# Kernel tuning notes

Hardware: AMD Instinct MI355X
Metric: run time of the kernel (lower is better)

Reference implementation:

```python
import jax, jax.numpy as jnp
import numpy as np

N = 50000      # nodes
E = 800000     # edges
DIM = 64       # node feature dim (= out_channels per head)
H = 4          # attention heads
EDGE_DIM = 3
LN_EPS = 1e-5
SLOPE = 0.2    # leaky relu negative slope (GATv2 default and FFN)


def _ln(x, g, b):
    mu = jnp.mean(x, axis=-1, keepdims=True)
    var = jnp.mean(jnp.square(x - mu), axis=-1, keepdims=True)
    return (x - mu) * jax.lax.rsqrt(var + LN_EPS) * g + b


def setup_inputs() -> dict:
    key = jax.random.key(0)
    ks = jax.random.split(key, 10)
    def g(k, shape, s=0.05):
        return jax.random.normal(k, shape, dtype=jnp.float32) * s
    return {
        "x": g(ks[0], (N, DIM), 1.0),
        "edge_index": jax.random.randint(ks[1], (2, E), 0, N),
        "edge_attr": g(ks[2], (E, EDGE_DIM), 1.0),
        # GATv2Conv params (lin_l, lin_r with bias; lin_edge no bias; att; out bias)
        "Wl": g(ks[3], (DIM, H * DIM)), "bl": jnp.zeros((H * DIM,), jnp.float32),
        "Wr": g(ks[4], (DIM, H * DIM)), "br": jnp.zeros((H * DIM,), jnp.float32),
        "We": g(ks[5], (EDGE_DIM, H * DIM)),
        "att_w": g(ks[6], (H, DIM)),
        "gat_b": jnp.zeros((DIM,), jnp.float32),
        # LayerNorms
        "ln1_g": jnp.ones((DIM,), jnp.float32), "ln1_b": jnp.zeros((DIM,), jnp.float32),
        "ln2_g": jnp.ones((DIM,), jnp.float32), "ln2_b": jnp.zeros((DIM,), jnp.float32),
        # FFN
        "W1": g(ks[7], (DIM, 2 * DIM)), "b1": jnp.zeros((2 * DIM,), jnp.float32),
        "W2": g(ks[8], (2 * DIM, DIM)), "b2": jnp.zeros((DIM,), jnp.float32),
    }


def _gatv2(x, edge_index, edge_attr, Wl, bl, Wr, br, We, att_w, gat_b):
    n = x.shape[0]
    src, dst = edge_index[0], edge_index[1]
    # add self loops; edge_attr fill_value='mean' (PyG default): per-target mean
    ea_sum = jax.ops.segment_sum(edge_attr, dst, num_segments=n)
    cnt = jax.ops.segment_sum(jnp.ones((edge_attr.shape[0], 1), edge_attr.dtype), dst, num_segments=n)
    loop_attr = ea_sum / jnp.maximum(cnt, 1.0)
    loop = jnp.arange(n)
    src = jnp.concatenate([src, loop])
    dst = jnp.concatenate([dst, loop])
    ea = jnp.concatenate([edge_attr, loop_attr], axis=0)
    # projections: [N,H,C]
    xl = (x @ Wl + bl).reshape(n, H, DIM)
    xr = (x @ Wr + br).reshape(n, H, DIM)
    ee = (ea @ We).reshape(-1, H, DIM)      # [E+N,H,C]
    z = jax.nn.leaky_relu(xl[src] + xr[dst] + ee, SLOPE)
    logits = jnp.einsum('ehc,hc->eh', z, att_w)   # [E+N,H]
    m = jax.ops.segment_max(logits, dst, num_segments=n)
    e = jnp.exp(logits - m[dst])
    denom = jax.ops.segment_sum(e, dst, num_segments=n)
    alpha = e / denom[dst]                         # segment softmax over targets
    out = jax.ops.segment_sum(alpha[:, :, None] * xl[src], dst, num_segments=n)
    return out.mean(axis=1) + gat_b               # concat=False -> head mean


def reference(x, edge_index, edge_attr, Wl, bl, Wr, br, We, att_w, gat_b,
              ln1_g, ln1_b, ln2_g, ln2_b, W1, b1, W2, b2):
    h = x + _gatv2(x, edge_index, edge_attr, Wl, bl, Wr, br, We, att_w, gat_b)
    h = _ln(h, ln1_g, ln1_b)
    ffn = jax.nn.leaky_relu(h @ W1 + b1, SLOPE) @ W2 + b2
    h = _ln(h + ffn, ln2_g, ln2_b)
    return h
```

## Files before the change

### kernel.cpp

```cpp
#include <hip/hip_runtime.h>
#include <hip/hip_fp16.h>

#ifndef __has_builtin
#define __has_builtin(x) 0
#endif

#define N_NODES 50000
#define N_EDGES 800000
#define DIM 64
#define NH 4
#define LN_EPS 1e-5f
#define SLOPE 0.2f
#define LOG2E 1.44269504f
#define PBLOCKS 782
#define BCAP 64

typedef _Float16 half4v __attribute__((ext_vector_type(4)));
typedef float floatx4 __attribute__((ext_vector_type(4)));

__device__ __forceinline__ float lrelu(float v){ return v > 0.f ? v : SLOPE * v; }

__device__ __forceinline__ float waveSum64(float v){
  v += __shfl_xor(v, 1);  v += __shfl_xor(v, 2);  v += __shfl_xor(v, 4);
  v += __shfl_xor(v, 8);  v += __shfl_xor(v, 16); v += __shfl_xor(v, 32);
  return v;
}

__device__ __forceinline__ __half2 u2h2(unsigned u){ union{unsigned u; __half2 h;} c; c.u = u; return c.h; }
__device__ __forceinline__ unsigned h22u(__half2 h){ union{unsigned u; __half2 h;} c; c.h = h; return c.u; }

__device__ __forceinline__ __half2 hmax2(__half2 a, __half2 b){
  unsigned ua = h22u(a), ub = h22u(b), r;
  asm("v_pk_max_f16 %0, %1, %2" : "=v"(r) : "v"(ua), "v"(ub));
  return u2h2(r);
}

__device__ __forceinline__ float fdot2f(unsigned a, unsigned b, float c){
#if __has_builtin(__builtin_amdgcn_fdot2)
  typedef _Float16 h2v __attribute__((ext_vector_type(2)));
  union U{unsigned u; h2v h;};
  U ua, ub; ua.u = a; ub.u = b;
  return __builtin_amdgcn_fdot2(ua.h, ub.h, c, false);
#else
  float r;
  asm("v_dot2_f32_f16 %0, %1, %2, %3" : "=v"(r) : "v"(a), "v"(b), "v"(c));
  return r;
#endif
}

__device__ __forceinline__ float exp2fast(float x){
#if __has_builtin(__builtin_amdgcn_exp2f)
  return __builtin_amdgcn_exp2f(x);
#else
  float r; asm("v_exp_f32 %0, %1" : "=v"(r) : "v"(x)); return r;
#endif
}

__device__ __forceinline__ float sum16fast(float v){
  asm("s_nop 1\n\t"
      "v_add_f32_dpp %0, %0, %0 quad_perm:[1,0,3,2] row_mask:0xf bank_mask:0xf\n\t"
      "s_nop 1\n\t"
      "v_add_f32_dpp %0, %0, %0 quad_perm:[2,3,0,1] row_mask:0xf bank_mask:0xf\n\t"
      "s_nop 1\n\t"
      "v_add_f32_dpp %0, %0, %0 row_ror:4 row_mask:0xf bank_mask:0xf\n\t"
      "s_nop 1\n\t"
      "v_add_f32_dpp %0, %0, %0 row_ror:8 row_mask:0xf bank_mask:0xf"
      : "+v"(v));
  return v;
}

__device__ __forceinline__ void sum16quad(float& a, float& b, float& c, float& d){
  asm("v_add_f32_dpp %0, %0, %0 quad_perm:[1,0,3,2] row_mask:0xf bank_mask:0xf\n\t"
      "v_add_f32_dpp %1, %1, %1 quad_perm:[1,0,3,2] row_mask:0xf bank_mask:0xf\n\t"
      "v_add_f32_dpp %2, %2, %2 quad_perm:[1,0,3,2] row_mask:0xf bank_mask:0xf\n\t"
      "v_add_f32_dpp %3, %3, %3 quad_perm:[1,0,3,2] row_mask:0xf bank_mask:0xf\n\t"
      "v_add_f32_dpp %0, %0, %0 quad_perm:[2,3,0,1] row_mask:0xf bank_mask:0xf\n\t"
      "v_add_f32_dpp %1, %1, %1 quad_perm:[2,3,0,1] row_mask:0xf bank_mask:0xf\n\t"
      "v_add_f32_dpp %2, %2, %2 quad_perm:[2,3,0,1] row_mask:0xf bank_mask:0xf\n\t"
      "v_add_f32_dpp %3, %3, %3 quad_perm:[2,3,0,1] row_mask:0xf bank_mask:0xf\n\t"
      "v_add_f32_dpp %0, %0, %0 row_ror:4 row_mask:0xf bank_mask:0xf\n\t"
      "v_add_f32_dpp %1, %1, %1 row_ror:4 row_mask:0xf bank_mask:0xf\n\t"
      "v_add_f32_dpp %2, %2, %2 row_ror:4 row_mask:0xf bank_mask:0xf\n\t"
      "v_add_f32_dpp %3, %3, %3 row_ror:4 row_mask:0xf bank_mask:0xf\n\t"
      "v_add_f32_dpp %0, %0, %0 row_ror:8 row_mask:0xf bank_mask:0xf\n\t"
      "v_add_f32_dpp %1, %1, %1 row_ror:8 row_mask:0xf bank_mask:0xf\n\t"
      "v_add_f32_dpp %2, %2, %2 row_ror:8 row_mask:0xf bank_mask:0xf\n\t"
      "v_add_f32_dpp %3, %3, %3 row_ror:8 row_mask:0xf bank_mask:0xf"
      : "+v"(a), "+v"(b), "+v"(c), "+v"(d));
}

__global__ __launch_bounds__(256)
void proj_kernel(const float* __restrict__ x,
                 const float* __restrict__ Wl, const float* __restrict__ bl,
                 const float* __restrict__ Wr, const float* __restrict__ br,
                 __half* __restrict__ xlh, __half* __restrict__ xrh,
                 const int* __restrict__ ei, const float* __restrict__ ea,
                 int* __restrict__ cursor, uint2* __restrict__ buckets,
                 const float* __restrict__ W1, const float* __restrict__ W2,
                 unsigned* __restrict__ W1p, unsigned* __restrict__ W2p){
  __shared__ __half ot[16][512];
  const int tid = threadIdx.x;
  const int lane = tid & 63, w = tid >> 6;
  const int row = lane & 15, kg = lane >> 4;

  const int gid0 = blockIdx.x * 256 + tid;
  if (gid0 < 4096){
    int kk = gid0 >> 7, cc = gid0 & 127;
    W1p[gid0] = h22u(__floats2half2_rn(W1[(2 * kk) * 128 + cc], W1[(2 * kk + 1) * 128 + cc]));
  } else if (gid0 < 8192){
    int j = gid0 - 4096;
    int kk = j >> 6, cc = j & 63;
    W2p[j] = h22u(__floats2half2_rn(W2[(2 * kk) * 64 + cc], W2[(2 * kk + 1) * 64 + cc]));
  }

  int edst[4], epos[4]; uint2 epk[4]; bool ehas[4];
#pragma unroll
  for (int q = 0; q < 4; ++q){
    const int e = gid0 + q * (PBLOCKS * 256);
    ehas[q] = e < N_EDGES;
    const int ec = ehas[q] ? e : 0;
    edst[q] = ei[N_EDGES + ec];
    const int src = ei[ec];
    const float e0 = ea[ec * 3 + 0], e1 = ea[ec * 3 + 1], e2 = ea[ec * 3 + 2];
    epk[q].x = h22u(__floats2half2_rn(e0, e1));
    epk[q].y = (h22u(__floats2half2_rn(e2, 0.f)) & 0xffffu) | ((unsigned)src << 16);
    epos[q] = ehas[q] ? atomicAdd(&cursor[edst[q]], 1) : 0;
  }

  const int colb = w * 128;
  const bool isL = colb < 256;
  const float* Wb = isL ? Wl : Wr;
  const float* bb = isL ? bl : br;
  const int cl = colb & 255;
  half4v bf[8][4];
  float bias[8];
#pragma unroll
  for (int nt = 0; nt < 8; ++nt){
    const int c = cl + nt * 16 + row;
    bias[nt] = bb[c];
#pragma unroll
    for (int kc = 0; kc < 4; ++kc){
      half4v b;
#pragma unroll
      for (int e = 0; e < 4; ++e)
        b[e] = (_Float16)Wb[(kc * 16 + kg * 4 + e) * 256 + c];
      bf[nt][kc] = b;
    }
  }

  const int nbase = blockIdx.x * 64;
  for (int m = 0; m < 4; ++m){
    const int nb = nbase + m * 16;
    if (nb >= N_NODES) break;
    const int nld = min(nb + row, N_NODES - 1);
    half4v af[4];
#pragma unroll
    for (int kc = 0; kc < 4; ++kc){
      const float4 xv = *(const float4*)&x[(size_t)nld * 64 + kc * 16 + kg * 4];
      half4v a;
      a[0] = (_Float16)xv.x; a[1] = (_Float16)xv.y;
      a[2] = (_Float16)xv.z; a[3] = (_Float16)xv.w;
      af[kc] = a;
    }
    __syncthreads();
#pragma unroll
    for (int nt = 0; nt < 8; ++nt){
      floatx4 acc = {0.f, 0.f, 0.f, 0.f};
      acc = __builtin_amdgcn_mfma_f32_16x16x16f16(af[0], bf[nt][0], acc, 0, 0, 0);
      acc = __builtin_amdgcn_mfma_f32_16x16x16f16(af[1], bf[nt][1], acc, 0, 0, 0);
      acc = __builtin_amdgcn_mfma_f32_16x16x16f16(af[2], bf[nt][2], acc, 0, 0, 0);
      acc = __builtin_amdgcn_mfma_f32_16x16x16f16(af[3], bf[nt][3], acc, 0, 0, 0);
      const int c = w * 128 + nt * 16 + row;
#pragma unroll
      for (int r = 0; r < 4; ++r)
        ot[kg * 4 + r][c] = __float2half(acc[r] + bias[nt]);
    }
    __syncthreads();
#pragma unroll
    for (int s = 0; s < 4; ++s){
      const int idx = s * 256 + tid;
      const int r = idx >> 6, q = idx & 63;
      const int n = nb + r;
      if (n < N_NODES){
        const uint4 v = *(const uint4*)&ot[r][q * 8];
        if (q < 32) *(uint4*)(xlh + (size_t)n * 256 + q * 8) = v;
        else        *(uint4*)(xrh + (size_t)n * 256 + (q - 32) * 8) = v;
      }
    }
  }

#pragma unroll
  for (int q = 0; q < 4; ++q){
    if (ehas[q]){
      const int p = min(epos[q], BCAP - 1);
      buckets[(size_t)edst[q] * BCAP + p] = epk[q];
    }
  }
}

#define EDGE_MATH(he0, he1, he2, a01, a23, p)                                        \
  {                                                                                  \
    __half2 z01 = __hadd2(a01, xr01);                                                \
    z01 = __hfma2(u2h2(he0), w0a, z01);                                              \
    z01 = __hfma2(u2h2(he1), w1a, z01);                                              \
    z01 = __hfma2(u2h2(he2), w2a, z01);                                              \
    __half2 z23 = __hadd2(a23, xr23);                                                \
    z23 = __hfma2(u2h2(he0), w0b, z23);                                              \
    z23 = __hfma2(u2h2(he1), w1b, z23);                                              \
    z23 = __hfma2(u2h2(he2), w2b, z23);                                              \
    z01 = hmax2(z01, __hmul2(z01, slp));                                             \
    z23 = hmax2(z23, __hmul2(z23, slp));                                             \
    p = fdot2f(h22u(z01), awa, fdot2f(h22u(z23), awb, 0.f));                         \
  }

__global__ __launch_bounds__(64)
void aggregate_kernel(const int* __restrict__ cursor, const uint2* __restrict__ buckets,
                      const __half* __restrict__ xlh, const __half* __restrict__ xrh,
                      const float* __restrict__ We, const float* __restrict__ att,
                      const float* __restrict__ x, const float* __restrict__ gat_b,
                      const float* __restrict__ ln1g, const float* __restrict__ ln1b,
                      __half* __restrict__ h1h){
  const int n = blockIdx.x;
  const int lane = threadIdx.x;
  const int j0 = lane * 4;
  const unsigned awa = h22u(__floats2half2_rn(att[j0] * LOG2E, att[j0 + 1] * LOG2E));
  const unsigned awb = h22u(__floats2half2_rn(att[j0 + 2] * LOG2E, att[j0 + 3] * LOG2E));
  const __half2 w0a = __floats2half2_rn(We[j0], We[j0 + 1]);
  const __half2 w0b = __floats2half2_rn(We[j0 + 2], We[j0 + 3]);
  const __half2 w1a = __floats2half2_rn(We[256 + j0], We[256 + j0 + 1]);
  const __half2 w1b = __floats2half2_rn(We[256 + j0 + 2], We[256 + j0 + 3]);
  const __half2 w2a = __floats2half2_rn(We[512 + j0], We[512 + j0 + 1]);
  const __half2 w2b = __floats2half2_rn(We[512 + j0 + 2], We[512 + j0 + 3]);
  const __half2 slp = __float2half2_rn(SLOPE);
  uint2 uxr = *(const uint2*)(xrh + (size_t)n * 256 + j0);
  const __half2 xr01 = u2h2(uxr.x), xr23 = u2h2(uxr.y);

  __half2 acc01 = __float2half2_rn(0.f), acc23 = __float2half2_rn(0.f);
  float den = 0.f;
  const int deg = min(cursor[n], BCAP);
  uint2 m2; m2.x = 0; m2.y = 0;
  if (lane < deg) m2 = buckets[(size_t)n * BCAP + lane];
  float s0 = __low2float(u2h2(m2.x));
  float s1 = __high2float(u2h2(m2.x));
  float s2 = __low2float(u2h2(m2.y & 0xffffu));
  int j = 0;
  for (; j + 4 <= deg; j += 4){
    const unsigned sxA = (unsigned)__builtin_amdgcn_readlane((int)m2.x, j);
    const unsigned syA = (unsigned)__builtin_amdgcn_readlane((int)m2.y, j);
    const unsigned sxB = (unsigned)__builtin_amdgcn_readlane((int)m2.x, j + 1);
    const unsigned syB = (unsigned)__builtin_amdgcn_readlane((int)m2.y, j + 1);
    const unsigned sxC = (unsigned)__builtin_amdgcn_readlane((int)m2.x, j + 2);
    const unsigned syC = (unsigned)__builtin_amdgcn_readlane((int)m2.y, j + 2);
    const unsigned sxD = (unsigned)__builtin_amdgcn_readlane((int)m2.x, j + 3);
    const unsigned syD = (unsigned)__builtin_amdgcn_readlane((int)m2.y, j + 3);
    uint2 uA = *(const uint2*)(xlh + (size_t)(syA >> 16) * 256 + j0);
    uint2 uB = *(const uint2*)(xlh + (size_t)(syB >> 16) * 256 + j0);
    uint2 uC = *(const uint2*)(xlh + (size_t)(syC >> 16) * 256 + j0);
    uint2 uD = *(const uint2*)(xlh + (size_t)(syD >> 16) * 256 + j0);
    const unsigned heA0 = (sxA & 0xffffu) | (sxA << 16), heA1 = (sxA >> 16) | (sxA & 0xffff0000u), heA2 = (syA & 0xffffu) | (syA << 16);
    const unsigned heB0 = (sxB & 0xffffu) | (sxB << 16), heB1 = (sxB >> 16) | (sxB & 0xffff0000u), heB2 = (syB & 0xffffu) | (syB << 16);
    const unsigned heC0 = (sxC & 0xffffu) | (sxC << 16), heC1 = (sxC >> 16) | (sxC & 0xffff0000u), heC2 = (syC & 0xffffu) | (syC << 16);
    const unsigned heD0 = (sxD & 0xffffu) | (sxD << 16), heD1 = (sxD >> 16) | (sxD & 0xffff0000u), heD2 = (syD & 0xffffu) | (syD << 16);
    const __half2 aA01 = u2h2(uA.x), aA23 = u2h2(uA.y);
    const __half2 aB01 = u2h2(uB.x), aB23 = u2h2(uB.y);
    const __half2 aC01 = u2h2(uC.x), aC23 = u2h2(uC.y);
    const __half2 aD01 = u2h2(uD.x), aD23 = u2h2(uD.y);
    float pA, pB, pC, pD;
    EDGE_MATH(heA0, heA1, heA2, aA01, aA23, pA)
    EDGE_MATH(heB0, heB1, heB2, aB01, aB23, pB)
    EDGE_MATH(heC0, heC1, heC2, aC01, aC23, pC)
    EDGE_MATH(heD0, heD1, heD2, aD01, aD23, pD)
    sum16quad(pA, pB, pC, pD);
    float wA = exp2fast(pA), wB = exp2fast(pB);
    float wC = exp2fast(pC), wD = exp2fast(pD);
    __half2 whA = __float2half2_rn(wA), whB = __float2half2_rn(wB);
    __half2 whC = __float2half2_rn(wC), whD = __float2half2_rn(wD);
    acc01 = __hfma2(whA, aA01, acc01); acc23 = __hfma2(whA, aA23, acc23);
    acc01 = __hfma2(whB, aB01, acc01); acc23 = __hfma2(whB, aB23, acc23);
    acc01 = __hfma2(whC, aC01, acc01); acc23 = __hfma2(whC, aC23, acc23);
    acc01 = __hfma2(whD, aD01, acc01); acc23 = __hfma2(whD, aD23, acc23);
    den += (wA + wB) + (wC + wD);
  }
  for (; j < deg; ++j){
    const unsigned sx = (unsigned)__builtin_amdgcn_readlane((int)m2.x, j);
    const unsigned sy = (unsigned)__builtin_amdgcn_readlane((int)m2.y, j);
    const unsigned he0 = (sx & 0xffffu) | (sx << 16);
    const unsigned he1 = (sx >> 16) | (sx & 0xffff0000u);
    const unsigned he2 = (sy & 0xffffu) | (sy << 16);
    uint2 u = *(const uint2*)(xlh + (size_t)(sy >> 16) * 256 + j0);
    const __half2 a01 = u2h2(u.x), a23 = u2h2(u.y);
    float p;
    EDGE_MATH(he0, he1, he2, a01, a23, p)
    p = sum16fast(p);
    float w = exp2fast(p);
    __half2 wh = __float2half2_rn(w);
    acc01 = __hfma2(wh, a01, acc01);
    acc23 = __hfma2(wh, a23, acc23);
    den += w;
  }

  {
    const float inv = 1.f / (float)max(deg, 1);
    const float e0 = waveSum64(s0) * inv;
    const float e1 = waveSum64(s1) * inv;
    const float e2 = waveSum64(s2) * inv;
    const __half2 he0h = __float2half2_rn(e0), he1h = __float2half2_rn(e1), he2h = __float2half2_rn(e2);
    uint2 u = *(const uint2*)(xlh + (size_t)n * 256 + j0);
    const __half2 a01 = u2h2(u.x), a23 = u2h2(u.y);
    __half2 z01 = __hadd2(a01, xr01);
    z01 = __hfma2(he0h, w0a, z01); z01 = __hfma2(he1h, w1a, z01); z01 = __hfma2(he2h, w2a, z01);
    __half2 z23 = __hadd2(a23, xr23);
    z23 = __hfma2(he0h, w0b, z23); z23 = __hfma2(he1h, w1b, z23); z23 = __hfma2(he2h, w2b, z23);
    z01 = hmax2(z01, __hmul2(z01, slp));
    z23 = hmax2(z23, __hmul2(z23, slp));
    float p = fdot2f(h22u(z01), awa, fdot2f(h22u(z23), awb, 0.f));
    p = sum16fast(p);
    float w = exp2fast(p);
    __half2 wh = __float2half2_rn(w);
    acc01 = __hfma2(wh, a01, acc01);
    acc23 = __hfma2(wh, a23, acc23);
    den += w;
  }

  float rd = 1.f / den;
  float4 o;
  o.x = __low2float(acc01) * rd; o.y = __high2float(acc01) * rd;
  o.z = __low2float(acc23) * rd; o.w = __high2float(acc23) * rd;
  o.x += __shfl_xor(o.x, 16); o.x += __shfl_xor(o.x, 32);
  o.y += __shfl_xor(o.y, 16); o.y += __shfl_xor(o.y, 32);
  o.z += __shfl_xor(o.z, 16); o.z += __shfl_xor(o.z, 32);
  o.w += __shfl_xor(o.w, 16); o.w += __shfl_xor(o.w, 32);
  const int c0 = (lane & 15) * 4;
  const float4 xv = *(const float4*)(x + (size_t)n * 64 + c0);
  const float4 gb = *(const float4*)(gat_b + c0);
  o.x = 0.25f * o.x + gb.x + xv.x;
  o.y = 0.25f * o.y + gb.y + xv.y;
  o.z = 0.25f * o.z + gb.z + xv.z;
  o.w = 0.25f * o.w + gb.w + xv.w;
  float t1 = sum16fast(o.x + o.y + o.z + o.w);
  float mu = t1 * (1.f / 64.f);
  float4 d; d.x = o.x - mu; d.y = o.y - mu; d.z = o.z - mu; d.w = o.w - mu;
  float t2 = sum16fast(d.x * d.x + d.y * d.y + d.z * d.z + d.w * d.w);
  float rs = rsqrtf(t2 * (1.f / 64.f) + LN_EPS);
  if (lane < 16){
    const float4 g4 = *(const float4*)(ln1g + c0);
    const float4 b4 = *(const float4*)(ln1b + c0);
    uint2 r;
    r.x = h22u(__floats2half2_rn(d.x * rs * g4.x + b4.x, d.y * rs * g4.y + b4.y));
    r.y = h22u(__floats2half2_rn(d.z * rs * g4.z + b4.z, d.w * rs * g4.w + b4.w));
    *(uint2*)(h1h + (size_t)n * 64 + c0) = r;
  }
}

#define FT 32
__global__ void ffn_kernel(const __half* __restrict__ h1h,
                           const unsigned* __restrict__ W1p, const float* __restrict__ b1,
                           const unsigned* __restrict__ W2p, const float* __restrict__ b2,
                           const float* __restrict__ ln2g, const float* __restrict__ ln2b,
                           float* __restrict__ out){
  __shared__ __half2 hs2[FT][32];
  __shared__ __half  ts1[FT][128];
  __shared__ float   fs[FT][64];
  const int base = blockIdx.x * FT;
  const int tid = threadIdx.x;
  for (int i = tid; i < FT * 32; i += 256){
    int r = i >> 5, cc = i & 31;
    int n = base + r;
    unsigned hu = 0;
    if (n < N_NODES) hu = ((const unsigned*)(h1h + (size_t)n * 64))[cc];
    __half2 hv = u2h2(hu);
    hs2[r][cc] = hv;
    fs[r][cc * 2] = __low2float(hv); fs[r][cc * 2 + 1] = __high2float(hv);
  }
  __syncthreads();
  {
    const int c1 = tid & 127, half = tid >> 7;
    __half2 acc[16];
#pragma unroll
    for (int i = 0; i < 16; ++i) acc[i] = __float2half2_rn(0.f);
    for (int kk = 0; kk < 32; kk += 2){
      __half2 wA = u2h2(W1p[(kk + 0) * 128 + c1]);
      __half2 wB = u2h2(W1p[(kk + 1) * 128 + c1]);
#pragma unroll
      for (int i = 0; i < 16; ++i){
        uint2 hv = *(const uint2*)&hs2[half * 16 + i][kk];
        acc[i] = __hfma2(u2h2(hv.x), wA, acc[i]);
        acc[i] = __hfma2(u2h2(hv.y), wB, acc[i]);
      }
    }
    const float b1c = b1[c1];
#pragma unroll
    for (int i = 0; i < 16; ++i){
      float t = __low2float(acc[i]) + __high2float(acc[i]) + b1c;
      ts1[half * 16 + i][c1] = __float2half(lrelu(t));
    }
  }
  __syncthreads();
  {
    const int c2 = tid & 63, qq = tid >> 6;
    __half2 acc2[8];
#pragma unroll
    for (int i = 0; i < 8; ++i) acc2[i] = __float2half2_rn(0.f);
    for (int kk = 0; kk < 64; kk += 2){
      __half2 wA = u2h2(W2p[(kk + 0) * 64 + c2]);
      __half2 wB = u2h2(W2p[(kk + 1) * 64 + c2]);
#pragma unroll
      for (int i = 0; i < 8; ++i){
        uint2 tt = *(const uint2*)&ts1[qq * 8 + i][2 * kk];
        acc2[i] = __hfma2(u2h2(tt.x), wA, acc2[i]);
        acc2[i] = __hfma2(u2h2(tt.y), wB, acc2[i]);
      }
    }
    const float b2c = b2[c2];
#pragma unroll
    for (int i = 0; i < 8; ++i)
      fs[qq * 8 + i][c2] += __low2float(acc2[i]) + __high2float(acc2[i]) + b2c;
  }
  __syncthreads();
  {
    const int lane = tid & 63, qq = tid >> 6;
    const float g = ln2g[lane], bb = ln2b[lane];
    for (int i = 0; i < 8; ++i){
      int r = qq * 8 + i;
      int n = base + r;
      if (n >= N_NODES) break;
      float v = fs[r][lane];
      float mu = waveSum64(v) * (1.f / 64.f);
      float dlt = v - mu;
      float var = waveSum64(dlt * dlt) * (1.f / 64.f);
      out[(size_t)n * 64 + lane] = dlt * rsqrtf(var + LN_EPS) * g + bb;
    }
  }
}

extern "C" void kernel_launch(void* const* d_in, const int* in_sizes, int n_in,
                              void* d_out, int out_size, void* d_ws, size_t ws_size,
                              hipStream_t stream){
  const float* x     = (const float*)d_in[0];
  const int*   ei    = (const int*)  d_in[1];
  const float* ea    = (const float*)d_in[2];
  const float* Wl    = (const float*)d_in[3];
  const float* bl    = (const float*)d_in[4];
  const float* Wr    = (const float*)d_in[5];
  const float* br    = (const float*)d_in[6];
  const float* We    = (const float*)d_in[7];
  const float* att   = (const float*)d_in[8];
  const float* gat_b = (const float*)d_in[9];
  const float* ln1g  = (const float*)d_in[10];
  const float* ln1b  = (const float*)d_in[11];
  const float* ln2g  = (const float*)d_in[12];
  const float* ln2b  = (const float*)d_in[13];
  const float* W1    = (const float*)d_in[14];
  const float* b1    = (const float*)d_in[15];
  const float* W2    = (const float*)d_in[16];
  const float* b2    = (const float*)d_in[17];
  float* out = (float*)d_out;

  uint2*    buckets = (uint2*)d_ws;
  __half*   xlh     = (__half*)(buckets + (size_t)N_NODES * BCAP);
  __half*   xrh     = xlh + (size_t)N_NODES * 256;
  __half*   h1h     = xrh + (size_t)N_NODES * 256;
  int*      cursor  = (int*)(h1h + (size_t)N_NODES * 64);
  unsigned* W1p     = (unsigned*)(cursor + N_NODES);
  unsigned* W2p     = W1p + 4096;

  (void)hipMemsetAsync(cursor, 0, (size_t)N_NODES * sizeof(int), stream);

  proj_kernel<<<PBLOCKS, 256, 0, stream>>>(x, Wl, bl, Wr, br, xlh, xrh,
                                           ei, ea, cursor, buckets, W1, W2, W1p, W2p);
  aggregate_kernel<<<N_NODES, 64, 0, stream>>>(
      cursor, buckets, xlh, xrh, We, att, x, gat_b, ln1g, ln1b, h1h);
  ffn_kernel<<<(N_NODES + FT - 1) / FT, 256, 0, stream>>>(h1h, W1p, b1, W2p, b2, ln2g, ln2b, out);
}
```

Baseline: 163.0 us.

## Split edge bucketing out of projection kernel into separate fill kernel

Moves the edge bucket fill (atomic cursor increments, packing edge attributes and source index) and the FFN weight packing out of the MFMA projection kernel into a new one-thread-per-edge fill kernel that runs first. The projection kernel then only does the GEMM, with fewer live registers and a padded shared-memory tile row (520 instead of 512) to reduce bank conflicts. This gives up the overlap of atomic latency with MFMA work and adds one kernel launch plus a serialization point between the two phases.

```diff
diff --git a/kernel.cpp b/kernel.cpp
--- a/kernel.cpp
+++ b/kernel.cpp
@@ -89,43 +89,40 @@
       : "+v"(a), "+v"(b), "+v"(c), "+v"(d));
 }
 
+__global__ void fill_kernel(const int* __restrict__ ei, const float* __restrict__ ea,
+                            int* __restrict__ cursor, uint2* __restrict__ buckets,
+                            const float* __restrict__ W1, const float* __restrict__ W2,
+                            unsigned* __restrict__ W1p, unsigned* __restrict__ W2p){
+  const int gid = blockIdx.x * blockDim.x + threadIdx.x;
+  if (gid < 4096){
+    int kk = gid >> 7, cc = gid & 127;
+    W1p[gid] = h22u(__floats2half2_rn(W1[(2 * kk) * 128 + cc], W1[(2 * kk + 1) * 128 + cc]));
+  } else if (gid < 8192){
+    int j = gid - 4096;
+    int kk = j >> 6, cc = j & 63;
+    W2p[j] = h22u(__floats2half2_rn(W2[(2 * kk) * 64 + cc], W2[(2 * kk + 1) * 64 + cc]));
+  }
+  if (gid >= N_EDGES) return;
+  const int dst = ei[N_EDGES + gid];
+  const int src = ei[gid];
+  const float e0 = ea[gid * 3 + 0], e1 = ea[gid * 3 + 1], e2 = ea[gid * 3 + 2];
+  int pos = atomicAdd(&cursor[dst], 1);
+  pos = min(pos, BCAP - 1);
+  uint2 v;
+  v.x = h22u(__floats2half2_rn(e0, e1));
+  v.y = (h22u(__floats2half2_rn(e2, 0.f)) & 0xffffu) | ((unsigned)src << 16);
+  buckets[(size_t)dst * BCAP + pos] = v;
+}
+
 __global__ __launch_bounds__(256)
 void proj_kernel(const float* __restrict__ x,
                  const float* __restrict__ Wl, const float* __restrict__ bl,
                  const float* __restrict__ Wr, const float* __restrict__ br,
-                 __half* __restrict__ xlh, __half* __restrict__ xrh,
-                 const int* __restrict__ ei, const float* __restrict__ ea,
-                 int* __restrict__ cursor, uint2* __restrict__ buckets,
-                 const float* __restrict__ W1, const float* __restrict__ W2,
-                 unsigned* __restrict__ W1p, unsigned* __restrict__ W2p){
-  __shared__ __half ot[16][512];
+                 __half* __restrict__ xlh, __half* __restrict__ xrh){
+  __shared__ __half ot[16][520];
   const int tid = threadIdx.x;
   const int lane = tid & 63, w = tid >> 6;
   const int row = lane & 15, kg = lane >> 4;
-
-  const int gid0 = blockIdx.x * 256 + tid;
-  if (gid0 < 4096){
-    int kk = gid0 >> 7, cc = gid0 & 127;
-    W1p[gid0] = h22u(__floats2half2_rn(W1[(2 * kk) * 128 + cc], W1[(2 * kk + 1) * 128 + cc]));
-  } else if (gid0 < 8192){
-    int j = gid0 - 4096;
-    int kk = j >> 6, cc = j & 63;
-    W2p[j] = h22u(__floats2half2_rn(W2[(2 * kk) * 64 + cc], W2[(2 * kk + 1) * 64 + cc]));
-  }
-
-  int edst[4], epos[4]; uint2 epk[4]; bool ehas[4];
-#pragma unroll
-  for (int q = 0; q < 4; ++q){
-    const int e = gid0 + q * (PBLOCKS * 256);
-    ehas[q] = e < N_EDGES;
-    const int ec = ehas[q] ? e : 0;
-    edst[q] = ei[N_EDGES + ec];
-    const int src = ei[ec];
-    const float e0 = ea[ec * 3 + 0], e1 = ea[ec * 3 + 1], e2 = ea[ec * 3 + 2];
-    epk[q].x = h22u(__floats2half2_rn(e0, e1));
-    epk[q].y = (h22u(__floats2half2_rn(e2, 0.f)) & 0xffffu) | ((unsigned)src << 16);
-    epos[q] = ehas[q] ? atomicAdd(&cursor[edst[q]], 1) : 0;
-  }
 
   const int colb = w * 128;
   const bool isL = colb < 256;
@@ -186,14 +183,6 @@
         if (q < 32) *(uint4*)(xlh + (size_t)n * 256 + q * 8) = v;
         else        *(uint4*)(xrh + (size_t)n * 256 + (q - 32) * 8) = v;
       }
-    }
-  }
-
-#pragma unroll
-  for (int q = 0; q < 4; ++q){
-    if (ehas[q]){
-      const int p = min(epos[q], BCAP - 1);
-      buckets[(size_t)edst[q] * BCAP + p] = epk[q];
     }
   }
 }
@@ -466,8 +455,8 @@
 
   (void)hipMemsetAsync(cursor, 0, (size_t)N_NODES * sizeof(int), stream);
 
-  proj_kernel<<<PBLOCKS, 256, 0, stream>>>(x, Wl, bl, Wr, br, xlh, xrh,
-                                           ei, ea, cursor, buckets, W1, W2, W1p, W2p);
+  fill_kernel<<<(N_EDGES + 255) / 256, 256, 0, stream>>>(ei, ea, cursor, buckets, W1, W2, W1p, W2p);
+  proj_kernel<<<PBLOCKS, 256, 0, stream>>>(x, Wl, bl, Wr, br, xlh, xrh);
   aggregate_kernel<<<N_NODES, 64, 0, stream>>>(
       cursor, buckets, xlh, xrh, We, att, x, gat_b, ln1g, ln1b, h1h);
   ffn_kernel<<<(N_NODES + FT - 1) / FT, 256, 0, stream>>>(h1h, W1p, b1, W2p, b2, ln2g, ln2b, out);
```

Result: slower. 179.2 us (+9.9%).
